# Optimization experiments

Hardware: AMD Instinct MI355X
Metric: run time of the kernel (lower is better)

The kernel has to match this reference:

```python
import jax, jax.numpy as jnp
import numpy as np

B, L, IN_DIM, OUT_DIM, N_BRANCH = 16, 1024, 300, 100, 60

def setup_inputs() -> dict:
    key = jax.random.key(0)
    ks = jax.random.split(key, 7)
    s = 0.05  # weight init scale
    return {
        "x": jax.random.normal(ks[0], (B, L, IN_DIM), dtype=jnp.float32),
        "W2": jax.random.normal(ks[1], (N_BRANCH, OUT_DIM, IN_DIM, 2), dtype=jnp.float32) * s,
        "b2": jax.random.normal(ks[2], (N_BRANCH, OUT_DIM), dtype=jnp.float32) * s,
        "W3": jax.random.normal(ks[3], (N_BRANCH, OUT_DIM, IN_DIM, 3), dtype=jnp.float32) * s,
        "b3": jax.random.normal(ks[4], (N_BRANCH, OUT_DIM), dtype=jnp.float32) * s,
        "W4": jax.random.normal(ks[5], (N_BRANCH, OUT_DIM, IN_DIM, 4), dtype=jnp.float32) * s,
        "b4": jax.random.normal(ks[6], (N_BRANCH, OUT_DIM), dtype=jnp.float32) * s,
    }

def _branch_group(xc, W, b):
    # xc: [B, C, L]; W: [n, o, c, k]; b: [n, o]
    # Batch all n same-kernel-size branches into ONE conv with n*o output channels.
    n, o, c, k = W.shape
    Wf = W.reshape(n * o, c, k)
    y = jax.lax.conv_general_dilated(
        xc, Wf, window_strides=(1,), padding="VALID",
        dimension_numbers=("NCH", "OIH", "NCH"))  # [B, n*o, L-k+1]
    y = jax.nn.relu(y + b.reshape(n * o)[None, :, None])
    y = jnp.max(y, axis=-1)                      # AdaptiveMaxPool1d(1): [B, n*o]
    # concat dim=2 in torch stacks branches along the length axis -> [B, o, n]
    return jnp.transpose(y.reshape(xc.shape[0], n, o), (0, 2, 1))

def reference(x, W2, b2, W3, b3, W4, b4):
    xc = jnp.transpose(x, (0, 2, 1))  # [B, in_dim, L]
    out = jnp.concatenate([
        _branch_group(xc, W2, b2),
        _branch_group(xc, W3, b3),
        _branch_group(xc, W4, b4),
    ], axis=2)                        # [B, out_dim, 180]
    # nn.Dropout(0.5) is identity in eval mode; omitted for the reference baseline.
    return out
```

## Files before the change

### kernel.cpp

```cpp
#include <hip/hip_runtime.h>
#include <cstdint>
#include <cstddef>

typedef unsigned short u16;
typedef unsigned int   u32;
typedef __attribute__((ext_vector_type(8))) short bf16x8;
typedef __attribute__((ext_vector_type(4))) float f32x4;

#define NB   16
#define LL   1024
#define CIN  300
#define CINP 320
#define XPBP (LL*CINP)
#define XELP (NB*XPBP)
#define NCH  6000
#define NCHP 6144
#define ODIM 100

#define BM 256
#define BN 256
#define BK 64

__device__ __forceinline__ u16 f2bf(float f) {
  union { float f; u32 u; } v; v.f = f;
  return (u16)((v.u + 0x7FFFu + ((v.u >> 16) & 1u)) >> 16);
}

typedef __attribute__((address_space(1))) const unsigned int gu32;
typedef __attribute__((address_space(3))) unsigned int lu32;
__device__ __forceinline__ void gload_lds16(const void* g, void* l) {
  __builtin_amdgcn_global_load_lds((gu32*)g, (lu32*)l, 16, 0, 0);
}

#define BAR() asm volatile("s_barrier" ::: "memory")

__global__ void cvt_x_kernel(const float* __restrict__ x, u16* __restrict__ xb) {
  int i8 = (blockIdx.x * 256 + threadIdx.x) * 8;
  int row = i8 / CINP;
  int col = i8 - row * CINP;
  const float* src = x + (size_t)row * CIN + col;
  u16 e[8];
  if (col + 8 <= CIN) {
    float4 a = *(const float4*)src;
    float4 b = *(const float4*)(src + 4);
    e[0]=f2bf(a.x); e[1]=f2bf(a.y); e[2]=f2bf(a.z); e[3]=f2bf(a.w);
    e[4]=f2bf(b.x); e[5]=f2bf(b.y); e[6]=f2bf(b.z); e[7]=f2bf(b.w);
  } else {
    #pragma unroll
    for (int j = 0; j < 8; j++)
      e[j] = (col + j < CIN) ? f2bf(src[j]) : (u16)0;
  }
  uint4 o;
  o.x = (u32)e[0] | ((u32)e[1] << 16);
  o.y = (u32)e[2] | ((u32)e[3] << 16);
  o.z = (u32)e[4] | ((u32)e[5] << 16);
  o.w = (u32)e[6] | ((u32)e[7] << 16);
  *(uint4*)(xb + i8) = o;
}

__global__ void repack_w_kernel(const float* __restrict__ W2, const float* __restrict__ W3,
                                const float* __restrict__ W4, u16* __restrict__ wb) {
  int g = blockIdx.y;
  int kk = g + 2;
  int Kp = kk * CINP;
  int woff = (g == 0) ? 0 : (g == 1) ? NCHP*640 : NCHP*(640+960);
  const float* W = (g == 0) ? W2 : (g == 1) ? W3 : W4;
  int no = blockIdx.x;
  u16* dst = wb + (size_t)woff + (size_t)no * Kp;
  const float* src = W + (size_t)no * (CIN * kk);
  for (int kp = threadIdx.x; kp < Kp; kp += 256) {
    int j = kp / CINP, c = kp - j * CINP;
    u16 v = 0;
    if (no < NCH && c < CIN) v = f2bf(src[c * kk + j]);
    dst[kp] = v;
  }
}

__global__ __launch_bounds__(512, 1)
void gemm_max_kernel(const u16* __restrict__ xb, const u16* __restrict__ wb,
                     const float* __restrict__ b2v, const float* __restrict__ b3v,
                     const float* __restrict__ b4v, float* __restrict__ out) {
  const int chblk = blockIdx.x;
  const int b     = blockIdx.y;
  const int g     = blockIdx.z;
  const int Kp    = (g + 2) * CINP;
  const int nks   = Kp >> 6;
  const int woff  = (g == 0) ? 0 : (g == 1) ? NCHP*640 : NCHP*(640+960);
  const int Lt    = LL - (g + 2) + 1;

  __shared__ __align__(16) u16 smem[4 * 16384];
  u16* A0s = smem;
  u16* B0s = smem + 16384;
  u16* A1s = smem + 32768;
  u16* B1s = smem + 49152;

  const int tid  = threadIdx.x;
  const int lane = tid & 63;
  const int w    = tid >> 6;
  const int wr   = w >> 2;
  const int wc   = w & 3;

  const u16* __restrict__ xrow = xb + (size_t)b * XPBP;
  const u16* __restrict__ Wg   = wb + (size_t)woff + (size_t)chblk * BN * Kp;

  auto STAGE = [&](const u16* src, int stride, u16* buf, int half) {
    #pragma unroll
    for (int i = 0; i < 2; i++) {
      int c = i * 512 + w * 64 + lane;
      int row128 = c >> 3;
      int colb = ((c & 7) * 16) ^ ((row128 & 7) << 4);
      gload_lds16(src + (size_t)(half * 128 + row128) * stride + (colb >> 1),
                  buf + half * 8192 + i * 4096 + w * 512);
    }
  };

  auto FR = [&](const u16* buf, int grp, int k) -> bf16x8 {
    int row  = grp * 16 + (lane & 15);
    int colb = (k * 64 + ((lane >> 4) << 4)) ^ ((lane & 7) << 4);
    return *(const bf16x8*)(buf + row * 64 + (colb >> 1));
  };

  f32x4 acc[8][4];
  #pragma unroll
  for (int mi = 0; mi < 8; mi++)
    #pragma unroll
    for (int ni = 0; ni < 4; ni++)
      acc[mi][ni] = (f32x4){0.f, 0.f, 0.f, 0.f};

  bf16x8 afr[4][2];
  bf16x8 bfr[2][2][2];
  float rmax[4] = { -1e30f, -1e30f, -1e30f, -1e30f };

  auto FOLD = [&](int ttf) {
    #pragma unroll
    for (int mi = 0; mi < 8; mi++) {
      int tb = ttf * 256 + (mi * 2 + wr) * 16 + ((lane >> 4) << 2);
      #pragma unroll
      for (int r = 0; r < 4; r++) {
        bool ok = (tb + r) < Lt;
        #pragma unroll
        for (int ni = 0; ni < 4; ni++)
          if (ok) rmax[ni] = fmaxf(rmax[ni], acc[mi][ni][r]);
      }
      #pragma unroll
      for (int ni = 0; ni < 4; ni++)
        acc[mi][ni] = (f32x4){0.f, 0.f, 0.f, 0.f};
    }
  };

#define PHASE(CA, CB, MHC, NH, RA, RB, STG, VM) do {                          \
    if (RA) {                                                                 \
      _Pragma("unroll")                                                       \
      for (int a2 = 0; a2 < 4; a2++) {                                        \
        _Pragma("unroll")                                                     \
        for (int k2 = 0; k2 < 2; k2++)                                        \
          afr[a2][k2] = FR(CA, ((MHC)*4 + a2) * 2 + wr, k2);                  \
      }                                                                       \
    }                                                                         \
    if (RB) {                                                                 \
      _Pragma("unroll")                                                       \
      for (int b2 = 0; b2 < 2; b2++) {                                        \
        _Pragma("unroll")                                                     \
        for (int k2 = 0; k2 < 2; k2++)                                        \
          bfr[NH][b2][k2] = FR(CB, ((NH)*2 + b2) * 4 + wc, k2);               \
      }                                                                       \
    }                                                                         \
    STG;                                                                      \
    BAR();                                                                    \
    __builtin_amdgcn_s_setprio(1);                                            \
    _Pragma("unroll")                                                         \
    for (int a2 = 0; a2 < 4; a2++)                                            \
      _Pragma("unroll")                                                       \
      for (int b2 = 0; b2 < 2; b2++)                                          \
        _Pragma("unroll")                                                     \
        for (int k2 = 0; k2 < 2; k2++)                                        \
          acc[(MHC)*4 + a2][(NH)*2 + b2] =                                    \
            __builtin_amdgcn_mfma_f32_16x16x32_bf16(afr[a2][k2],              \
              bfr[NH][b2][k2], acc[(MHC)*4 + a2][(NH)*2 + b2], 0, 0, 0);      \
    __builtin_amdgcn_s_setprio(0);                                            \
    VM;                                                                       \
    BAR();                                                                    \
  } while (0)

  const int NT = 4 * nks;
  int tt = 0, ks = 0;

  STAGE(xrow, CINP, A0s, 0);
  STAGE(Wg,   Kp,   B0s, 0);
  STAGE(Wg,   Kp,   B0s, 1);
  STAGE(xrow, CINP, A0s, 1);
  asm volatile("s_waitcnt vmcnt(4)" ::: "memory");
  BAR();

  for (int s = 0; s < NT - 1; s++) {
    int ks2 = ks + 1, tt2 = tt;
    if (ks2 == nks) { ks2 = 0; tt2++; }
    const u16* sA = xrow + (size_t)tt2 * (256 * CINP) + ks2 * 64;
    const u16* sB = Wg + ks2 * 64;
    u16* cA = (s & 1) ? A1s : A0s;
    u16* cB = (s & 1) ? B1s : B0s;
    u16* nA = (s & 1) ? A0s : A1s;
    u16* nB = (s & 1) ? B0s : B1s;

    PHASE(cA, cB, 0, 0, 1, 1, STAGE(sA, CINP, nA, 0),
          asm volatile("s_waitcnt vmcnt(4)" ::: "memory"));
    PHASE(cA, cB, 0, 1, 0, 1, STAGE(sB, Kp,   nB, 0),
          asm volatile("s_waitcnt vmcnt(4)" ::: "memory"));
    PHASE(cA, cB, 1, 0, 1, 0, STAGE(sB, Kp,   nB, 1),
          ((void)0));
    PHASE(cA, cB, 1, 1, 0, 0, STAGE(sA, CINP, nA, 1),
          asm volatile("s_waitcnt vmcnt(4) lgkmcnt(0)" ::: "memory"));

    if (++ks == nks) { FOLD(tt); ks = 0; tt++; }
  }

  {
    u16* cA = A1s;
    u16* cB = B1s;
    PHASE(cA, cB, 0, 0, 1, 1, ((void)0),
          asm volatile("s_waitcnt vmcnt(2)" ::: "memory"));
    PHASE(cA, cB, 0, 1, 0, 1, ((void)0),
          asm volatile("s_waitcnt vmcnt(0)" ::: "memory"));
    PHASE(cA, cB, 1, 0, 1, 0, ((void)0), ((void)0));
    PHASE(cA, cB, 1, 1, 0, 0, ((void)0),
          asm volatile("s_waitcnt lgkmcnt(0)" ::: "memory"));
    FOLD(tt);
  }
#undef PHASE

  float cv[4];
  #pragma unroll
  for (int ni = 0; ni < 4; ni++) {
    float v = rmax[ni];
    v = fmaxf(v, __shfl_xor(v, 16));
    v = fmaxf(v, __shfl_xor(v, 32));
    cv[ni] = v;
  }
  __syncthreads();
  float* red = (float*)smem;
  if (lane < 16) {
    #pragma unroll
    for (int ni = 0; ni < 4; ni++)
      red[wr * 256 + (ni * 4 + wc) * 16 + lane] = cv[ni];
  }
  __syncthreads();
  const float* bias = (g == 0) ? b2v : (g == 1) ? b3v : b4v;
  if (tid < 256) {
    float v = fmaxf(red[tid], red[256 + tid]);
    int ch = chblk * BN + tid;
    if (ch < NCH) {
      int n = ch / ODIM, o = ch - n * ODIM;
      out[b * (ODIM * 180) + o * 180 + g * 60 + n] = fmaxf(v + bias[ch], 0.f);
    }
  }
}

extern "C" void kernel_launch(void* const* d_in, const int* in_sizes, int n_in,
                              void* d_out, int out_size, void* d_ws, size_t ws_size,
                              hipStream_t stream) {
  const float* x  = (const float*)d_in[0];
  const float* W2 = (const float*)d_in[1];
  const float* b2 = (const float*)d_in[2];
  const float* W3 = (const float*)d_in[3];
  const float* b3 = (const float*)d_in[4];
  const float* W4 = (const float*)d_in[5];
  const float* b4 = (const float*)d_in[6];
  float* out = (float*)d_out;

  u16* xb = (u16*)d_ws;
  u16* wb = xb + XELP;

  cvt_x_kernel<<<XELP / (256 * 8), 256, 0, stream>>>(x, xb);
  repack_w_kernel<<<dim3(NCHP, 3), 256, 0, stream>>>(W2, W3, W4, wb);
  gemm_max_kernel<<<dim3(NCHP / BN, NB, 3), 512, 0, stream>>>(xb, wb, b2, b3, b4, out);
}
```

Before: 557.8 us.

## Split time axis across blocks with atomicMax combine and use 32x32 MFMA

Doubles the grid by splitting each sequence into two time halves handled by separate blocks, ordered so the largest-K group launches first, and combines partial maxima via atomicMax on float bits after zeroing the output. Switches the matrix core instruction from 16x16x32 to 32x32x16 bf16, reducing LDS fragment reads per flop, and drops the shared-memory cross-wave reduction. Intends to reduce tail imbalance and LDS traffic, at the cost of an extra zeroing kernel and global atomics.

Measured after the change: 604.4 us. +8.4%, slower.

```diff
diff --git a/kernel.cpp b/kernel.cpp
--- a/kernel.cpp
+++ b/kernel.cpp
@@ -4,8 +4,8 @@
 
 typedef unsigned short u16;
 typedef unsigned int   u32;
-typedef __attribute__((ext_vector_type(8))) short bf16x8;
-typedef __attribute__((ext_vector_type(4))) float f32x4;
+typedef __attribute__((ext_vector_type(8)))  short bf16x8;
+typedef __attribute__((ext_vector_type(16))) float f32x16;
 
 #define NB   16
 #define LL   1024
@@ -16,6 +16,7 @@
 #define NCH  6000
 #define NCHP 6144
 #define ODIM 100
+#define OUTN (NB*ODIM*180)
 
 #define BM 256
 #define BN 256
@@ -33,6 +34,11 @@
 }
 
 #define BAR() asm volatile("s_barrier" ::: "memory")
+
+__global__ void zero_out_kernel(float* __restrict__ out) {
+  int i = blockIdx.x * 256 + threadIdx.x;
+  if (i < OUTN) out[i] = 0.f;
+}
 
 __global__ void cvt_x_kernel(const float* __restrict__ x, u16* __restrict__ xb) {
   int i8 = (blockIdx.x * 256 + threadIdx.x) * 8;
@@ -80,9 +86,13 @@
 void gemm_max_kernel(const u16* __restrict__ xb, const u16* __restrict__ wb,
                      const float* __restrict__ b2v, const float* __restrict__ b3v,
                      const float* __restrict__ b4v, float* __restrict__ out) {
-  const int chblk = blockIdx.x;
-  const int b     = blockIdx.y;
-  const int g     = blockIdx.z;
+  const int id  = blockIdx.x;
+  const int g   = (id < 768) ? 2 : (id < 1536) ? 1 : 0;
+  const int id2 = id - ((g == 2) ? 0 : (g == 1) ? 768 : 1536);
+  const int b     = id2 / 48;
+  const int rem   = id2 - b * 48;
+  const int chblk = rem >> 1;
+  const int tpair = rem & 1;
   const int Kp    = (g + 2) * CINP;
   const int nks   = Kp >> 6;
   const int woff  = (g == 0) ? 0 : (g == 1) ? NCHP*640 : NCHP*(640+960);
@@ -114,88 +124,88 @@
     }
   };
 
-  auto FR = [&](const u16* buf, int grp, int k) -> bf16x8 {
-    int row  = grp * 16 + (lane & 15);
-    int colb = (k * 64 + ((lane >> 4) << 4)) ^ ((lane & 7) << 4);
+  auto FR32 = [&](const u16* buf, int grp, int ksl) -> bf16x8 {
+    int row  = grp * 32 + (lane & 31);
+    int colb = (ksl * 32 + ((lane >> 5) << 4)) ^ ((lane & 7) << 4);
     return *(const bf16x8*)(buf + row * 64 + (colb >> 1));
   };
 
-  f32x4 acc[8][4];
+  f32x16 acc[4][2];
   #pragma unroll
-  for (int mi = 0; mi < 8; mi++)
-    #pragma unroll
-    for (int ni = 0; ni < 4; ni++)
-      acc[mi][ni] = (f32x4){0.f, 0.f, 0.f, 0.f};
-
-  bf16x8 afr[4][2];
-  bf16x8 bfr[2][2][2];
-  float rmax[4] = { -1e30f, -1e30f, -1e30f, -1e30f };
-
-  auto FOLD = [&](int ttf) {
-    #pragma unroll
-    for (int mi = 0; mi < 8; mi++) {
-      int tb = ttf * 256 + (mi * 2 + wr) * 16 + ((lane >> 4) << 2);
+  for (int a2 = 0; a2 < 4; a2++)
+    #pragma unroll
+    for (int b2 = 0; b2 < 2; b2++)
       #pragma unroll
-      for (int r = 0; r < 4; r++) {
-        bool ok = (tb + r) < Lt;
+      for (int q = 0; q < 16; q++)
+        acc[a2][b2][q] = 0.f;
+
+  bf16x8 afr[2][4];
+  bf16x8 bfr[2][4];
+  float rmax[2] = { -1e30f, -1e30f };
+
+  auto FOLD = [&](int ttg) {
+    #pragma unroll
+    for (int a2 = 0; a2 < 4; a2++) {
+      int rowbase = ttg * 256 + (a2 * 2 + wr) * 32 + ((lane >> 5) << 2);
+      #pragma unroll
+      for (int r = 0; r < 16; r++) {
+        int t = rowbase + (r & 3) + 8 * (r >> 2);
+        bool ok = t < Lt;
         #pragma unroll
-        for (int ni = 0; ni < 4; ni++)
-          if (ok) rmax[ni] = fmaxf(rmax[ni], acc[mi][ni][r]);
+        for (int b2 = 0; b2 < 2; b2++) {
+          if (ok) rmax[b2] = fmaxf(rmax[b2], acc[a2][b2][r]);
+          acc[a2][b2][r] = 0.f;
+        }
       }
-      #pragma unroll
-      for (int ni = 0; ni < 4; ni++)
-        acc[mi][ni] = (f32x4){0.f, 0.f, 0.f, 0.f};
     }
   };
 
 #define PHASE(CA, CB, MHC, NH, RA, RB, STG, VM) do {                          \
     if (RA) {                                                                 \
       _Pragma("unroll")                                                       \
-      for (int a2 = 0; a2 < 4; a2++) {                                        \
+      for (int a2l = 0; a2l < 2; a2l++) {                                     \
         _Pragma("unroll")                                                     \
-        for (int k2 = 0; k2 < 2; k2++)                                        \
-          afr[a2][k2] = FR(CA, ((MHC)*4 + a2) * 2 + wr, k2);                  \
+        for (int ksl = 0; ksl < 4; ksl++)                                     \
+          afr[a2l][ksl] = FR32(CA, ((MHC)*2 + a2l) * 2 + wr, ksl);            \
       }                                                                       \
     }                                                                         \
     if (RB) {                                                                 \
       _Pragma("unroll")                                                       \
-      for (int b2 = 0; b2 < 2; b2++) {                                        \
-        _Pragma("unroll")                                                     \
-        for (int k2 = 0; k2 < 2; k2++)                                        \
-          bfr[NH][b2][k2] = FR(CB, ((NH)*2 + b2) * 4 + wc, k2);               \
-      }                                                                       \
+      for (int ksl = 0; ksl < 4; ksl++)                                       \
+        bfr[NH][ksl] = FR32(CB, (NH)*4 + wc, ksl);                            \
     }                                                                         \
     STG;                                                                      \
     BAR();                                                                    \
     __builtin_amdgcn_s_setprio(1);                                            \
     _Pragma("unroll")                                                         \
-    for (int a2 = 0; a2 < 4; a2++)                                            \
+    for (int ksl = 0; ksl < 4; ksl++)                                         \
       _Pragma("unroll")                                                       \
-      for (int b2 = 0; b2 < 2; b2++)                                          \
-        _Pragma("unroll")                                                     \
-        for (int k2 = 0; k2 < 2; k2++)                                        \
-          acc[(MHC)*4 + a2][(NH)*2 + b2] =                                    \
-            __builtin_amdgcn_mfma_f32_16x16x32_bf16(afr[a2][k2],              \
-              bfr[NH][b2][k2], acc[(MHC)*4 + a2][(NH)*2 + b2], 0, 0, 0);      \
+      for (int a2l = 0; a2l < 2; a2l++)                                       \
+        acc[(MHC)*2 + a2l][NH] =                                              \
+          __builtin_amdgcn_mfma_f32_32x32x16_bf16(afr[a2l][ksl],              \
+            bfr[NH][ksl], acc[(MHC)*2 + a2l][NH], 0, 0, 0);                   \
     __builtin_amdgcn_s_setprio(0);                                            \
     VM;                                                                       \
     BAR();                                                                    \
   } while (0)
 
-  const int NT = 4 * nks;
+  const int NT = 2 * nks;
   int tt = 0, ks = 0;
 
-  STAGE(xrow, CINP, A0s, 0);
-  STAGE(Wg,   Kp,   B0s, 0);
-  STAGE(Wg,   Kp,   B0s, 1);
-  STAGE(xrow, CINP, A0s, 1);
+  {
+    const u16* sA0 = xrow + (size_t)(tpair * 2) * (256 * CINP);
+    STAGE(sA0, CINP, A0s, 0);
+    STAGE(Wg,  Kp,   B0s, 0);
+    STAGE(Wg,  Kp,   B0s, 1);
+    STAGE(sA0, CINP, A0s, 1);
+  }
   asm volatile("s_waitcnt vmcnt(4)" ::: "memory");
   BAR();
 
   for (int s = 0; s < NT - 1; s++) {
     int ks2 = ks + 1, tt2 = tt;
     if (ks2 == nks) { ks2 = 0; tt2++; }
-    const u16* sA = xrow + (size_t)tt2 * (256 * CINP) + ks2 * 64;
+    const u16* sA = xrow + (size_t)(tpair * 2 + tt2) * (256 * CINP) + ks2 * 64;
     const u16* sB = Wg + ks2 * 64;
     u16* cA = (s & 1) ? A1s : A0s;
     u16* cB = (s & 1) ? B1s : B0s;
@@ -211,7 +221,7 @@
     PHASE(cA, cB, 1, 1, 0, 0, STAGE(sA, CINP, nA, 1),
           asm volatile("s_waitcnt vmcnt(4) lgkmcnt(0)" ::: "memory"));
 
-    if (++ks == nks) { FOLD(tt); ks = 0; tt++; }
+    if (++ks == nks) { FOLD(tpair * 2 + tt); ks = 0; tt++; }
   }
 
   {
@@ -224,33 +234,23 @@
     PHASE(cA, cB, 1, 0, 1, 0, ((void)0), ((void)0));
     PHASE(cA, cB, 1, 1, 0, 0, ((void)0),
           asm volatile("s_waitcnt lgkmcnt(0)" ::: "memory"));
-    FOLD(tt);
+    FOLD(tpair * 2 + tt);
   }
 #undef PHASE
 
-  float cv[4];
+  const float* bias = (g == 0) ? b2v : (g == 1) ? b3v : b4v;
   #pragma unroll
-  for (int ni = 0; ni < 4; ni++) {
-    float v = rmax[ni];
-    v = fmaxf(v, __shfl_xor(v, 16));
+  for (int b2 = 0; b2 < 2; b2++) {
+    float v = rmax[b2];
     v = fmaxf(v, __shfl_xor(v, 32));
-    cv[ni] = v;
-  }
-  __syncthreads();
-  float* red = (float*)smem;
-  if (lane < 16) {
-    #pragma unroll
-    for (int ni = 0; ni < 4; ni++)
-      red[wr * 256 + (ni * 4 + wc) * 16 + lane] = cv[ni];
-  }
-  __syncthreads();
-  const float* bias = (g == 0) ? b2v : (g == 1) ? b3v : b4v;
-  if (tid < 256) {
-    float v = fmaxf(red[tid], red[256 + tid]);
-    int ch = chblk * BN + tid;
-    if (ch < NCH) {
-      int n = ch / ODIM, o = ch - n * ODIM;
-      out[b * (ODIM * 180) + o * 180 + g * 60 + n] = fmaxf(v + bias[ch], 0.f);
+    if (lane < 32) {
+      int ch = chblk * BN + (b2 * 4 + wc) * 32 + lane;
+      if (ch < NCH) {
+        int n = ch / ODIM, o = ch - n * ODIM;
+        float r = fmaxf(v + bias[ch], 0.f);
+        atomicMax((u32*)&out[b * (ODIM * 180) + o * 180 + g * 60 + n],
+                  __float_as_uint(r));
+      }
     }
   }
 }
@@ -270,7 +270,8 @@
   u16* xb = (u16*)d_ws;
   u16* wb = xb + XELP;
 
+  zero_out_kernel<<<(OUTN + 255) / 256, 256, 0, stream>>>(out);
   cvt_x_kernel<<<XELP / (256 * 8), 256, 0, stream>>>(x, xb);
   repack_w_kernel<<<dim3(NCHP, 3), 256, 0, stream>>>(W2, W3, W4, wb);
-  gemm_max_kernel<<<dim3(NCHP / BN, NB, 3), 512, 0, stream>>>(xb, wb, b2, b3, b4, out);
-}
+  gemm_max_kernel<<<dim3(2304), 512, 0, stream>>>(xb, wb, b2, b3, b4, out);
+}
```
